# Optimization experiments

Measured on AMD Instinct MI355X. Metric: run time of the kernel, lower is better.

## Reference

```python
import jax, jax.numpy as jnp
import numpy as np

N_NODES = 50000
N_REL = 1000
N_EDGES = 600000
D = 128
DEPTH = 2


def setup_inputs() -> dict:
    key = jax.random.key(0)
    ks = jax.random.split(key, 10)
    features = jax.random.normal(ks[0], (N_NODES, D), dtype=jnp.float32)
    rel_emb = jax.random.normal(ks[1], (N_REL, D), dtype=jnp.float32)
    # edge list: row0 = destination (sorted, matches coalesced sparse layout), row1 = source
    dst = jnp.sort(jax.random.randint(ks[2], (N_EDGES,), 0, N_NODES))
    src = jax.random.randint(ks[3], (N_EDGES,), 0, N_NODES)
    adj = jnp.stack([dst, src]).astype(jnp.int64)
    # one relation entry per triple: r_index[0]=triple id, r_index[1]=relation id
    r_index = jnp.stack([
        jnp.arange(N_EDGES, dtype=jnp.int64),
        jax.random.randint(ks[4], (N_EDGES,), 0, N_REL).astype(jnp.int64),
    ])
    r_val = jax.random.uniform(ks[5], (N_EDGES,), dtype=jnp.float32)
    # Xavier-ish params
    attn_w = jax.random.normal(ks[6], (3 * D, 1), dtype=jnp.float32) * 0.05
    attn_b = jnp.zeros((1,), dtype=jnp.float32)
    gate_w = jax.random.normal(ks[7], (3 * D, 1), dtype=jnp.float32) * 0.05
    gate_b = jnp.zeros((1,), dtype=jnp.float32)
    attn_kernels = jax.random.normal(ks[8], (DEPTH, D, 1), dtype=jnp.float32) * (6.0 / (D + 1)) ** 0.5
    return {"features": features, "rel_emb": rel_emb, "adj": adj, "r_index": r_index,
            "r_val": r_val, "attn_w": attn_w, "attn_b": attn_b, "gate_w": gate_w,
            "gate_b": gate_b, "attn_kernels": attn_kernels}


def _segment_softmax(vals, seg, n):
    # numerically stable softmax over edges grouped by destination node `seg`
    m = jax.ops.segment_max(vals, seg, num_segments=n)
    e = jnp.exp(vals - m[seg])
    s = jax.ops.segment_sum(e, seg, num_segments=n)
    return e / s[seg]


def reference(features, rel_emb, adj, r_index, r_val, attn_w, attn_b, gate_w, gate_b, attn_kernels):
    n_nodes = features.shape[0]
    n_triples = adj.shape[1]
    depth = attn_kernels.shape[0]
    dst, src_idx = adj[0], adj[1]

    feats = jnp.tanh(features)
    outs_c = [feats]
    outs_s = [feats]

    for l in range(depth):
        # sparse [triple, rel] @ rel_emb -> per-triple relation embedding
        tri_rel = jax.ops.segment_sum(r_val[:, None] * rel_emb[r_index[1]], r_index[0],
                                      num_segments=n_triples)  # [E, D]
        tri_rel = tri_rel / jnp.maximum(
            jnp.linalg.norm(tri_rel, axis=1, keepdims=True), 1e-12)
        # gather neighbors and reflect through relation hyperplane
        neighs = feats[src_idx]  # [E, D]
        neighs = neighs - 2.0 * jnp.sum(neighs * tri_rel, axis=1, keepdims=True) * tri_rel
        # structural attention + row-wise sparse softmax
        att_struct = _segment_softmax((tri_rel @ attn_kernels[l])[:, 0], dst, n_nodes)
        feats = jnp.tanh(jax.ops.segment_sum(neighs * att_struct[:, None], dst,
                                             num_segments=n_nodes))
        outs_c.append(feats)
        # semantic branch on updated features
        neighs2 = feats[src_idx]
        source_emb = feats[dst]
        diff_raw = source_emb - neighs2
        att_input = jnp.concatenate([source_emb, neighs2, diff_raw], axis=-1)  # [E, 3D]
        att_score = jnp.maximum(jax.nn.sigmoid(att_input @ attn_w + attn_b)[:, 0], 1e-4)
        gate_score = jax.nn.sigmoid(att_input @ gate_w + gate_b)[:, 0]
        final_att = gate_score * att_score + (1.0 - gate_score) * att_struct
        att = _segment_softmax(final_att, dst, n_nodes)
        new_diff = jnp.tanh(jax.ops.segment_sum(diff_raw * att[:, None], dst,
                                                num_segments=n_nodes))
        outs_s.append(new_diff)

    return (jnp.concatenate(outs_c, axis=-1), jnp.concatenate(outs_s, axis=-1))
```

## Files before the change

### kernel.cpp

```cpp
#include <hip/hip_runtime.h>
#include <math.h>

#define N_NODES 50000
#define N_REL   1000
#define N_EDGES 600000
#define D       128
#define OUT_COLS 384

typedef unsigned short ushortT;

#define FEAT0_BLOCKS  ((N_NODES * (D / 4) + 255) / 256)
#define RELN_BLOCKS   ((N_REL + 3) / 4)
#define ROWPTR_BLOCKS ((N_NODES + 1 + 255) / 256)
#define SETUP_BLOCKS  (FEAT0_BLOCKS + RELN_BLOCKS + ROWPTR_BLOCKS + 1)

__device__ __forceinline__ float wave_reduce_sum64(float v) {
#pragma unroll
    for (int m = 1; m < 64; m <<= 1) v += __shfl_xor(v, m, 64);
    return v;
}

template <int CTRL>
__device__ __forceinline__ float dpp_add_(float v) {
    int t = __builtin_amdgcn_update_dpp(0, __float_as_int(v), CTRL, 0xf, 0xf, true);
    return v + __int_as_float(t);
}
__device__ __forceinline__ float group_sum16(float v) {
    v = dpp_add_<0xB1>(v);
    v = dpp_add_<0x4E>(v);
    v = dpp_add_<0x141>(v);
    v = dpp_add_<0x140>(v);
    return v;
}

__device__ __forceinline__ float tanh_fast(float x) {
    float cx = fminf(fmaxf(x, -20.0f), 20.0f);
    float e = __expf(2.0f * cx);
    return __fdividef(e - 1.0f, e + 1.0f);
}
__device__ __forceinline__ float sigmoid_fast(float x) {
    return __fdividef(1.0f, 1.0f + __expf(-x));
}

__device__ __forceinline__ void bf16x8_to_f32(uint4 q, float4& a, float4& b) {
    a.x = __int_as_float((int)(q.x << 16));
    a.y = __int_as_float((int)(q.x & 0xffff0000u));
    a.z = __int_as_float((int)(q.y << 16));
    a.w = __int_as_float((int)(q.y & 0xffff0000u));
    b.x = __int_as_float((int)(q.z << 16));
    b.y = __int_as_float((int)(q.z & 0xffff0000u));
    b.z = __int_as_float((int)(q.w << 16));
    b.w = __int_as_float((int)(q.w & 0xffff0000u));
}
__device__ __forceinline__ unsigned pack_bf16x2(float lo, float hi) {
    unsigned a = __float_as_uint(lo), b = __float_as_uint(hi);
    a = (a + 0x7fffu + ((a >> 16) & 1u)) >> 16;
    b = (b + 0x7fffu + ((b >> 16) & 1u));
    return (a & 0xffffu) | (b & 0xffff0000u);
}

__global__ __launch_bounds__(256) void k_setup(
        const float* __restrict__ features, const float* __restrict__ rel_emb,
        const float* __restrict__ attn_k, const float* __restrict__ attn_w,
        const float* __restrict__ gate_w, const int* __restrict__ dstv,
        float* __restrict__ out0, float* __restrict__ out1, ushortT* __restrict__ fc0,
        float* __restrict__ rel_norm, float* __restrict__ er0, float* __restrict__ er1,
        float* __restrict__ wcomb, int* __restrict__ row_ptr) {
    int bid = blockIdx.x, tid = threadIdx.x;
    if (bid < FEAT0_BLOCKS) {
        int i = bid * 256 + tid;
        if (i >= N_NODES * (D / 4)) return;
        int n = i >> 5, q = i & 31;
        float4 f = *(const float4*)(features + (size_t)n * D + 4 * q);
        f.x = tanh_fast(f.x); f.y = tanh_fast(f.y);
        f.z = tanh_fast(f.z); f.w = tanh_fast(f.w);
        *(float4*)(out0 + (size_t)n * OUT_COLS + 4 * q) = f;
        *(float4*)(out1 + (size_t)n * OUT_COLS + 4 * q) = f;
        uint2 p = make_uint2(pack_bf16x2(f.x, f.y), pack_bf16x2(f.z, f.w));
        *((uint2*)(fc0 + (size_t)n * D) + q) = p;
    } else if (bid < FEAT0_BLOCKS + RELN_BLOCKS) {
        int wid  = (bid - FEAT0_BLOCKS) * 4 + (tid >> 6);
        int lane = tid & 63;
        if (wid >= N_REL) return;
        float2 v = *(const float2*)(rel_emb + (size_t)wid * D + 2 * lane);
        float sq = wave_reduce_sum64(v.x * v.x + v.y * v.y);
        float inv = 1.0f / fmaxf(sqrtf(sq), 1e-12f);
        float2 u = make_float2(v.x * inv, v.y * inv);
        *(float2*)(rel_norm + (size_t)wid * D + 2 * lane) = u;
        float2 k0 = *(const float2*)(attn_k + 2 * lane);
        float2 k1 = *(const float2*)(attn_k + D + 2 * lane);
        float d0 = wave_reduce_sum64(u.x * k0.x + u.y * k0.y);
        float d1 = wave_reduce_sum64(u.x * k1.x + u.y * k1.y);
        if (lane == 0) { er0[wid] = __expf(d0); er1[wid] = __expf(d1); }
    } else if (bid < FEAT0_BLOCKS + RELN_BLOCKS + ROWPTR_BLOCKS) {
        int n = (bid - FEAT0_BLOCKS - RELN_BLOCKS) * 256 + tid;
        if (n > N_NODES) return;
        int lo = 0, hi = N_EDGES;
        while (lo < hi) {
            int mid = (lo + hi) >> 1;
            if (dstv[mid] < n) lo = mid + 1; else hi = mid;
        }
        row_ptr[n] = lo;
    } else {
        int j = tid;
        if (j >= D) return;
        wcomb[j]         = attn_w[j] + attn_w[2 * D + j];
        wcomb[D + j]     = attn_w[D + j] - attn_w[2 * D + j];
        wcomb[2 * D + j] = gate_w[j] + gate_w[2 * D + j];
        wcomb[3 * D + j] = gate_w[D + j] - gate_w[2 * D + j];
    }
}

__global__ __launch_bounds__(256) void k_struct(
        const ushortT* __restrict__ finC,
        ushortT* __restrict__ foutC,
        float* __restrict__ foutS,
        const int* __restrict__ row_ptr, const int* __restrict__ srcv,
        const int* __restrict__ relv, const float* __restrict__ rval,
        const float* __restrict__ er,
        const float* __restrict__ rel_norm, const float* __restrict__ wcomb,
        float* __restrict__ node_Z, float* __restrict__ proj) {
    int n    = (blockIdx.x * blockDim.x + threadIdx.x) >> 6;
    int lane = threadIdx.x & 63;
    int g = lane >> 4, l = lane & 15;
    if (n >= N_NODES) return;
    int beg = row_ptr[n], end = row_ptr[n + 1];

    float4 acc0 = make_float4(0.f, 0.f, 0.f, 0.f);
    float4 acc1 = make_float4(0.f, 0.f, 0.f, 0.f);
    float Zp = 0.f;

    for (int cs = beg; cs < end; cs += 64) {
        int cnt = min(64, end - cs);
        int my_s = 0, my_r = -1; float my_w = 0.f;
        if (lane < cnt) {
            int e = cs + lane;
            my_s = srcv[e];
            int rr = relv[e];
            bool pos = rval[e] > 0.0f;
            my_r = pos ? rr : -1;
            my_w = pos ? er[rr] : 1.0f;
            Zp += my_w;
        }
        int nit = (cnt + 3) >> 2;
        int   s = __shfl(my_s, g, 64);
        int   r = __shfl(my_r, g, 64);
        float w = __shfl(my_w, g, 64);
        uint4 xq = *((const uint4*)(finC + (size_t)s * D) + l);
        int rr0 = r < 0 ? 0 : r;
        const float* up = rel_norm + (size_t)rr0 * D + 8 * l;
        float4 u0 = *(const float4*)up;
        float4 u1 = *(const float4*)(up + 4);
        for (int i = 0; i < nit; ++i) {
            int r_c = r; float w_c = w;
            uint4 xq_c = xq; float4 u0_c = u0, u1_c = u1;
            if (i + 1 < nit) {
                int sl2 = ((i + 1) << 2) | g;
                s = __shfl(my_s, sl2, 64);
                r = __shfl(my_r, sl2, 64);
                w = __shfl(my_w, sl2, 64);
                xq = *((const uint4*)(finC + (size_t)s * D) + l);
                int rr2 = r < 0 ? 0 : r;
                const float* up2 = rel_norm + (size_t)rr2 * D + 8 * l;
                u0 = *(const float4*)up2;
                u1 = *(const float4*)(up2 + 4);
            }
            float4 x0, x1;
            bf16x8_to_f32(xq_c, x0, x1);
            float p = x0.x*u0_c.x + x0.y*u0_c.y + x0.z*u0_c.z + x0.w*u0_c.w
                    + x1.x*u1_c.x + x1.y*u1_c.y + x1.z*u1_c.z + x1.w*u1_c.w;
            p = group_sum16(p);
            float wc = (r_c >= 0) ? 2.0f * w_c * p : 0.0f;
            acc0.x += w_c * x0.x - wc * u0_c.x;
            acc0.y += w_c * x0.y - wc * u0_c.y;
            acc0.z += w_c * x0.z - wc * u0_c.z;
            acc0.w += w_c * x0.w - wc * u0_c.w;
            acc1.x += w_c * x1.x - wc * u1_c.x;
            acc1.y += w_c * x1.y - wc * u1_c.y;
            acc1.z += w_c * x1.z - wc * u1_c.z;
            acc1.w += w_c * x1.w - wc * u1_c.w;
        }
    }
    float Z = group_sum16(Zp);
    Z += __shfl_xor(Z, 16, 64);
    Z += __shfl_xor(Z, 32, 64);
#pragma unroll
    for (int m = 16; m < 64; m <<= 1) {
        acc0.x += __shfl_xor(acc0.x, m, 64);
        acc0.y += __shfl_xor(acc0.y, m, 64);
        acc0.z += __shfl_xor(acc0.z, m, 64);
        acc0.w += __shfl_xor(acc0.w, m, 64);
        acc1.x += __shfl_xor(acc1.x, m, 64);
        acc1.y += __shfl_xor(acc1.y, m, 64);
        acc1.z += __shfl_xor(acc1.z, m, 64);
        acc1.w += __shfl_xor(acc1.w, m, 64);
    }
    float invZ = (end > beg) ? (1.0f / Z) : 0.0f;
    float4 o0, o1;
    o0.x = tanh_fast(acc0.x * invZ); o0.y = tanh_fast(acc0.y * invZ);
    o0.z = tanh_fast(acc0.z * invZ); o0.w = tanh_fast(acc0.w * invZ);
    o1.x = tanh_fast(acc1.x * invZ); o1.y = tanh_fast(acc1.y * invZ);
    o1.z = tanh_fast(acc1.z * invZ); o1.w = tanh_fast(acc1.w * invZ);

    float pr[4];
#pragma unroll
    for (int k = 0; k < 4; ++k) {
        const float* wp = wcomb + k * D + 8 * l;
        float4 w0 = *(const float4*)wp;
        float4 w1 = *(const float4*)(wp + 4);
        float p = o0.x*w0.x + o0.y*w0.y + o0.z*w0.z + o0.w*w0.w
                + o1.x*w1.x + o1.y*w1.y + o1.z*w1.z + o1.w*w1.w;
        pr[k] = group_sum16(p);
    }
    if (lane == 0) {
        node_Z[n] = Z;
        *(float4*)(proj + 4 * (size_t)n) = make_float4(pr[0], pr[1], pr[2], pr[3]);
    }
    if (g == 0) {
        float* op = foutS + (size_t)n * OUT_COLS + 8 * l;
        *(float4*)op = o0;
        *(float4*)(op + 4) = o1;
        uint4 pk = make_uint4(pack_bf16x2(o0.x, o0.y), pack_bf16x2(o0.z, o0.w),
                              pack_bf16x2(o1.x, o1.y), pack_bf16x2(o1.z, o1.w));
        *((uint4*)(foutC + (size_t)n * D) + l) = pk;
    }
}

__global__ __launch_bounds__(256) void k_fused(
        const ushortT* __restrict__ finC,
        const float* __restrict__ seF,
        ushortT* __restrict__ foutC,
        float* __restrict__ foutS,
        float* __restrict__ oputSem,
        const int* __restrict__ row_ptr, const int* __restrict__ srcv,
        const int* __restrict__ relv, const float* __restrict__ rval,
        const float* __restrict__ er_sem,
        const float* __restrict__ er_st,
        const float* __restrict__ rel_norm, const float* __restrict__ wcomb,
        const float* __restrict__ node_Z0, const float* __restrict__ proj0,
        float* __restrict__ node_Z1, float* __restrict__ proj1,
        const float* __restrict__ attn_b, const float* __restrict__ gate_b) {
    int n    = (blockIdx.x * blockDim.x + threadIdx.x) >> 6;
    int lane = threadIdx.x & 63;
    int g = lane >> 4, l = lane & 15;
    if (n >= N_NODES) return;
    int beg = row_ptr[n], end = row_ptr[n + 1];

    float4 pn = *(const float4*)(proj0 + 4 * (size_t)n);
    float ca = pn.x + attn_b[0];
    float cg = pn.z + gate_b[0];
    float invZ0 = (end > beg) ? (1.0f / node_Z0[n]) : 0.0f;

    float4 st0 = make_float4(0.f, 0.f, 0.f, 0.f);
    float4 st1 = make_float4(0.f, 0.f, 0.f, 0.f);
    float4 sm0 = make_float4(0.f, 0.f, 0.f, 0.f);
    float4 sm1 = make_float4(0.f, 0.f, 0.f, 0.f);
    float Zp = 0.f, Zs = 0.f;

    for (int cs = beg; cs < end; cs += 64) {
        int cnt = min(64, end - cs);
        int my_s = 0, my_r = -1; float my_w = 0.f, my_wt = 0.f;
        if (lane < cnt) {
            int e = cs + lane;
            my_s = srcv[e];
            int rr = relv[e];
            bool pos = rval[e] > 0.0f;
            my_r = pos ? rr : -1;
            my_w = pos ? er_st[rr] : 1.0f;
            float sw = (pos ? er_sem[rr] : 1.0f) * invZ0;
            float4 ps = *(const float4*)(proj0 + 4 * (size_t)my_s);
            float as = fmaxf(sigmoid_fast(ca + ps.y), 1e-4f);
            float gt = sigmoid_fast(cg + ps.w);
            my_wt = __expf(gt * as + (1.0f - gt) * sw);
            Zp += my_w; Zs += my_wt;
        }
        int nit = (cnt + 3) >> 2;
        int   s  = __shfl(my_s, g, 64);
        int   r  = __shfl(my_r, g, 64);
        float w  = __shfl(my_w, g, 64);
        float wt = __shfl(my_wt, g, 64);
        uint4 xq = *((const uint4*)(finC + (size_t)s * D) + l);
        int rr0 = r < 0 ? 0 : r;
        const float* up = rel_norm + (size_t)rr0 * D + 8 * l;
        float4 u0 = *(const float4*)up;
        float4 u1 = *(const float4*)(up + 4);
        for (int i = 0; i < nit; ++i) {
            int r_c = r; float w_c = w, wt_c = wt;
            uint4 xq_c = xq; float4 u0_c = u0, u1_c = u1;
            if (i + 1 < nit) {
                int sl2 = ((i + 1) << 2) | g;
                s  = __shfl(my_s, sl2, 64);
                r  = __shfl(my_r, sl2, 64);
                w  = __shfl(my_w, sl2, 64);
                wt = __shfl(my_wt, sl2, 64);
                xq = *((const uint4*)(finC + (size_t)s * D) + l);
                int rr2 = r < 0 ? 0 : r;
                const float* up2 = rel_norm + (size_t)rr2 * D + 8 * l;
                u0 = *(const float4*)up2;
                u1 = *(const float4*)(up2 + 4);
            }
            float4 x0, x1;
            bf16x8_to_f32(xq_c, x0, x1);
            float p = x0.x*u0_c.x + x0.y*u0_c.y + x0.z*u0_c.z + x0.w*u0_c.w
                    + x1.x*u1_c.x + x1.y*u1_c.y + x1.z*u1_c.z + x1.w*u1_c.w;
            p = group_sum16(p);
            float wc = (r_c >= 0) ? 2.0f * w_c * p : 0.0f;
            st0.x += w_c * x0.x - wc * u0_c.x;
            st0.y += w_c * x0.y - wc * u0_c.y;
            st0.z += w_c * x0.z - wc * u0_c.z;
            st0.w += w_c * x0.w - wc * u0_c.w;
            st1.x += w_c * x1.x - wc * u1_c.x;
            st1.y += w_c * x1.y - wc * u1_c.y;
            st1.z += w_c * x1.z - wc * u1_c.z;
            st1.w += w_c * x1.w - wc * u1_c.w;
            sm0.x += wt_c * x0.x; sm0.y += wt_c * x0.y;
            sm0.z += wt_c * x0.z; sm0.w += wt_c * x0.w;
            sm1.x += wt_c * x1.x; sm1.y += wt_c * x1.y;
            sm1.z += wt_c * x1.z; sm1.w += wt_c * x1.w;
        }
    }
    float Z = group_sum16(Zp);
    Z += __shfl_xor(Z, 16, 64);
    Z += __shfl_xor(Z, 32, 64);
    float ZsT = group_sum16(Zs);
    ZsT += __shfl_xor(ZsT, 16, 64);
    ZsT += __shfl_xor(ZsT, 32, 64);
#pragma unroll
    for (int m = 16; m < 64; m <<= 1) {
        st0.x += __shfl_xor(st0.x, m, 64); st0.y += __shfl_xor(st0.y, m, 64);
        st0.z += __shfl_xor(st0.z, m, 64); st0.w += __shfl_xor(st0.w, m, 64);
        st1.x += __shfl_xor(st1.x, m, 64); st1.y += __shfl_xor(st1.y, m, 64);
        st1.z += __shfl_xor(st1.z, m, 64); st1.w += __shfl_xor(st1.w, m, 64);
        sm0.x += __shfl_xor(sm0.x, m, 64); sm0.y += __shfl_xor(sm0.y, m, 64);
        sm0.z += __shfl_xor(sm0.z, m, 64); sm0.w += __shfl_xor(sm0.w, m, 64);
        sm1.x += __shfl_xor(sm1.x, m, 64); sm1.y += __shfl_xor(sm1.y, m, 64);
        sm1.z += __shfl_xor(sm1.z, m, 64); sm1.w += __shfl_xor(sm1.w, m, 64);
    }
    float invZ = (end > beg) ? (1.0f / Z) : 0.0f;
    float4 o0, o1;
    o0.x = tanh_fast(st0.x * invZ); o0.y = tanh_fast(st0.y * invZ);
    o0.z = tanh_fast(st0.z * invZ); o0.w = tanh_fast(st0.w * invZ);
    o1.x = tanh_fast(st1.x * invZ); o1.y = tanh_fast(st1.y * invZ);
    o1.z = tanh_fast(st1.z * invZ); o1.w = tanh_fast(st1.w * invZ);

    float pr[4];
#pragma unroll
    for (int k = 0; k < 4; ++k) {
        const float* wp = wcomb + k * D + 8 * l;
        float4 w0 = *(const float4*)wp;
        float4 w1 = *(const float4*)(wp + 4);
        float p = o0.x*w0.x + o0.y*w0.y + o0.z*w0.z + o0.w*w0.w
                + o1.x*w1.x + o1.y*w1.y + o1.z*w1.z + o1.w*w1.w;
        pr[k] = group_sum16(p);
    }
    if (lane == 0) {
        node_Z1[n] = Z;
        *(float4*)(proj1 + 4 * (size_t)n) = make_float4(pr[0], pr[1], pr[2], pr[3]);
    }
    if (g == 0) {
        float* op = foutS + (size_t)n * OUT_COLS + 8 * l;
        *(float4*)op = o0;
        *(float4*)(op + 4) = o1;
        uint4 pk = make_uint4(pack_bf16x2(o0.x, o0.y), pack_bf16x2(o0.z, o0.w),
                              pack_bf16x2(o1.x, o1.y), pack_bf16x2(o1.z, o1.w));
        *((uint4*)(foutC + (size_t)n * D) + l) = pk;
        float invZs = (end > beg) ? (1.0f / ZsT) : 0.0f;
        float sc    = (end > beg) ? 1.0f : 0.0f;
        const float* sp = seF + (size_t)n * OUT_COLS + 8 * l;
        float4 s0 = *(const float4*)sp;
        float4 s1 = *(const float4*)(sp + 4);
        float4 q0, q1;
        q0.x = tanh_fast(sc * (s0.x - sm0.x * invZs));
        q0.y = tanh_fast(sc * (s0.y - sm0.y * invZs));
        q0.z = tanh_fast(sc * (s0.z - sm0.z * invZs));
        q0.w = tanh_fast(sc * (s0.w - sm0.w * invZs));
        q1.x = tanh_fast(sc * (s1.x - sm1.x * invZs));
        q1.y = tanh_fast(sc * (s1.y - sm1.y * invZs));
        q1.z = tanh_fast(sc * (s1.z - sm1.z * invZs));
        q1.w = tanh_fast(sc * (s1.w - sm1.w * invZs));
        float* oq = oputSem + (size_t)n * OUT_COLS + 8 * l;
        *(float4*)oq = q0;
        *(float4*)(oq + 4) = q1;
    }
}

__global__ __launch_bounds__(256) void k_sem(
        const ushortT* __restrict__ featsC,
        const float* __restrict__ seF,
        float* __restrict__ oput,
        const int* __restrict__ row_ptr, const int* __restrict__ srcv,
        const int* __restrict__ relv, const float* __restrict__ rval,
        const float* __restrict__ er, const float* __restrict__ node_Z,
        const float* __restrict__ proj,
        const float* __restrict__ attn_b, const float* __restrict__ gate_b) {
    int n    = (blockIdx.x * blockDim.x + threadIdx.x) >> 6;
    int lane = threadIdx.x & 63;
    int g = lane >> 4, l = lane & 15;
    if (n >= N_NODES) return;
    int beg = row_ptr[n], end = row_ptr[n + 1];

    float4 pn = *(const float4*)(proj + 4 * (size_t)n);
    float ca = pn.x + attn_b[0];
    float cg = pn.z + gate_b[0];
    float invZ = (end > beg) ? (1.0f / node_Z[n]) : 0.0f;

    float4 acc0 = make_float4(0.f, 0.f, 0.f, 0.f);
    float4 acc1 = make_float4(0.f, 0.f, 0.f, 0.f);
    float Zs = 0.f;

    for (int cs = beg; cs < end; cs += 64) {
        int cnt = min(64, end - cs);
        int my_s = 0; float my_wt = 0.f;
        if (lane < cnt) {
            int e = cs + lane;
            my_s = srcv[e];
            int rr = relv[e];
            bool pos = rval[e] > 0.0f;
            float sw = (pos ? er[rr] : 1.0f) * invZ;
            float4 ps = *(const float4*)(proj + 4 * (size_t)my_s);
            float as = fmaxf(sigmoid_fast(ca + ps.y), 1e-4f);
            float gt = sigmoid_fast(cg + ps.w);
            my_wt = __expf(gt * as + (1.0f - gt) * sw);
            Zs += my_wt;
        }
        int nit = (cnt + 3) >> 2;
        int   s  = __shfl(my_s, g, 64);
        float wt = __shfl(my_wt, g, 64);
        uint4 xq = *((const uint4*)(featsC + (size_t)s * D) + l);
        for (int i = 0; i < nit; ++i) {
            float wt_c = wt; uint4 xq_c = xq;
            if (i + 1 < nit) {
                int sl2 = ((i + 1) << 2) | g;
                s  = __shfl(my_s, sl2, 64);
                wt = __shfl(my_wt, sl2, 64);
                xq = *((const uint4*)(featsC + (size_t)s * D) + l);
            }
            float4 x0, x1;
            bf16x8_to_f32(xq_c, x0, x1);
            acc0.x += wt_c * x0.x; acc0.y += wt_c * x0.y;
            acc0.z += wt_c * x0.z; acc0.w += wt_c * x0.w;
            acc1.x += wt_c * x1.x; acc1.y += wt_c * x1.y;
            acc1.z += wt_c * x1.z; acc1.w += wt_c * x1.w;
        }
    }
    Zs = group_sum16(Zs);
    Zs += __shfl_xor(Zs, 16, 64);
    Zs += __shfl_xor(Zs, 32, 64);
#pragma unroll
    for (int m = 16; m < 64; m <<= 1) {
        acc0.x += __shfl_xor(acc0.x, m, 64);
        acc0.y += __shfl_xor(acc0.y, m, 64);
        acc0.z += __shfl_xor(acc0.z, m, 64);
        acc0.w += __shfl_xor(acc0.w, m, 64);
        acc1.x += __shfl_xor(acc1.x, m, 64);
        acc1.y += __shfl_xor(acc1.y, m, 64);
        acc1.z += __shfl_xor(acc1.z, m, 64);
        acc1.w += __shfl_xor(acc1.w, m, 64);
    }
    if (g == 0) {
        float invZs = (end > beg) ? (1.0f / Zs) : 0.0f;
        float sc    = (end > beg) ? 1.0f : 0.0f;
        const float* sp = seF + (size_t)n * OUT_COLS + 8 * l;
        float4 s0 = *(const float4*)sp;
        float4 s1 = *(const float4*)(sp + 4);
        float4 o0, o1;
        o0.x = tanh_fast(sc * (s0.x - acc0.x * invZs));
        o0.y = tanh_fast(sc * (s0.y - acc0.y * invZs));
        o0.z = tanh_fast(sc * (s0.z - acc0.z * invZs));
        o0.w = tanh_fast(sc * (s0.w - acc0.w * invZs));
        o1.x = tanh_fast(sc * (s1.x - acc1.x * invZs));
        o1.y = tanh_fast(sc * (s1.y - acc1.y * invZs));
        o1.z = tanh_fast(sc * (s1.z - acc1.z * invZs));
        o1.w = tanh_fast(sc * (s1.w - acc1.w * invZs));
        float* op = oput + (size_t)n * OUT_COLS + 8 * l;
        *(float4*)op = o0;
        *(float4*)(op + 4) = o1;
    }
}

extern "C" void kernel_launch(void* const* d_in, const int* in_sizes, int n_in,
                              void* d_out, int out_size, void* d_ws, size_t ws_size,
                              hipStream_t stream) {
    const float* features = (const float*)d_in[0];
    const float* rel_emb  = (const float*)d_in[1];
    const int*   adj      = (const int*)d_in[2];
    const int*   r_index  = (const int*)d_in[3];
    const float* r_val    = (const float*)d_in[4];
    const float* attn_w   = (const float*)d_in[5];
    const float* attn_b   = (const float*)d_in[6];
    const float* gate_w   = (const float*)d_in[7];
    const float* gate_b   = (const float*)d_in[8];
    const float* attn_k   = (const float*)d_in[9];

    float* out0 = (float*)d_out;
    float* out1 = out0 + (size_t)N_NODES * OUT_COLS;

    float* rel_norm = (float*)d_ws;
    float* er0      = rel_norm + (size_t)N_REL * D;
    float* er1      = er0 + N_REL;
    float* wcomb    = er1 + N_REL;
    float* proj0    = wcomb + 4 * D;
    float* proj1    = proj0 + 4 * (size_t)N_NODES;
    float* node_Z0  = proj1 + 4 * (size_t)N_NODES;
    float* node_Z1  = node_Z0 + N_NODES;
    int*   row_ptr  = (int*)(node_Z1 + N_NODES);
    ushortT* fc0    = (ushortT*)(row_ptr + N_NODES + 4);
    ushortT* fc1    = fc0 + (size_t)N_NODES * D;
    ushortT* fc2    = fc1 + (size_t)N_NODES * D;

    const int* dstv = adj;
    const int* srcv = adj + N_EDGES;
    const int* relv = r_index + N_EDGES;

    k_setup<<<SETUP_BLOCKS, 256, 0, stream>>>(
        features, rel_emb, attn_k, attn_w, gate_w, dstv,
        out0, out1, fc0, rel_norm, er0, er1, wcomb, row_ptr);

    k_struct<<<(N_NODES + 3) / 4, 256, 0, stream>>>(
        fc0, fc1, out0 + (size_t)1 * D,
        row_ptr, srcv, relv, r_val, er0, rel_norm, wcomb, node_Z0, proj0);

    k_fused<<<(N_NODES + 3) / 4, 256, 0, stream>>>(
        fc1, out0 + (size_t)1 * D, fc2, out0 + (size_t)2 * D, out1 + (size_t)1 * D,
        row_ptr, srcv, relv, r_val, er0, er1, rel_norm, wcomb,
        node_Z0, proj0, node_Z1, proj1, attn_b, gate_b);

    k_sem<<<(N_NODES + 3) / 4, 256, 0, stream>>>(
        fc2, out0 + (size_t)2 * D, out1 + (size_t)2 * D,
        row_ptr, srcv, relv, r_val, er1, node_Z1, proj1, attn_b, gate_b);
}
```

Baseline: 360.6 us.

## Fuse four kernels into one persistent kernel with software grid barriers

Replaces the setup, struct, fused and sem kernel launches with a single persistent kernel of 960 blocks. Each phase is processed with grid-stride loops over nodes, one wave per node, and the phases are separated by atomic-counter grid barriers. The intent is to remove kernel launch gaps and tail effects between dependent phases. The costs are spin-wait overhead, fixed occupancy limits, and a deadlock risk if all 960 blocks cannot be co-resident. An extra memset is needed to reset the barrier counters on every call.

Measured after the change: 1.244 ms. 245% more time.

```diff
diff --git a/kernel.cpp b/kernel.cpp
--- a/kernel.cpp
+++ b/kernel.cpp
@@ -7,12 +7,12 @@
 #define D       128
 #define OUT_COLS 384
 
+#define NBLOCKS  960
+#define NTHREADS 256
+#define NWAVES   (NBLOCKS * NTHREADS / 64)
+#define NTHR     (NBLOCKS * NTHREADS)
+
 typedef unsigned short ushortT;
-
-#define FEAT0_BLOCKS  ((N_NODES * (D / 4) + 255) / 256)
-#define RELN_BLOCKS   ((N_REL + 3) / 4)
-#define ROWPTR_BLOCKS ((N_NODES + 1 + 255) / 256)
-#define SETUP_BLOCKS  (FEAT0_BLOCKS + RELN_BLOCKS + ROWPTR_BLOCKS + 1)
 
 __device__ __forceinline__ float wave_reduce_sum64(float v) {
 #pragma unroll
@@ -59,71 +59,28 @@
     return (a & 0xffffu) | (b & 0xffff0000u);
 }
 
-__global__ __launch_bounds__(256) void k_setup(
-        const float* __restrict__ features, const float* __restrict__ rel_emb,
-        const float* __restrict__ attn_k, const float* __restrict__ attn_w,
-        const float* __restrict__ gate_w, const int* __restrict__ dstv,
-        float* __restrict__ out0, float* __restrict__ out1, ushortT* __restrict__ fc0,
-        float* __restrict__ rel_norm, float* __restrict__ er0, float* __restrict__ er1,
-        float* __restrict__ wcomb, int* __restrict__ row_ptr) {
-    int bid = blockIdx.x, tid = threadIdx.x;
-    if (bid < FEAT0_BLOCKS) {
-        int i = bid * 256 + tid;
-        if (i >= N_NODES * (D / 4)) return;
-        int n = i >> 5, q = i & 31;
-        float4 f = *(const float4*)(features + (size_t)n * D + 4 * q);
-        f.x = tanh_fast(f.x); f.y = tanh_fast(f.y);
-        f.z = tanh_fast(f.z); f.w = tanh_fast(f.w);
-        *(float4*)(out0 + (size_t)n * OUT_COLS + 4 * q) = f;
-        *(float4*)(out1 + (size_t)n * OUT_COLS + 4 * q) = f;
-        uint2 p = make_uint2(pack_bf16x2(f.x, f.y), pack_bf16x2(f.z, f.w));
-        *((uint2*)(fc0 + (size_t)n * D) + q) = p;
-    } else if (bid < FEAT0_BLOCKS + RELN_BLOCKS) {
-        int wid  = (bid - FEAT0_BLOCKS) * 4 + (tid >> 6);
-        int lane = tid & 63;
-        if (wid >= N_REL) return;
-        float2 v = *(const float2*)(rel_emb + (size_t)wid * D + 2 * lane);
-        float sq = wave_reduce_sum64(v.x * v.x + v.y * v.y);
-        float inv = 1.0f / fmaxf(sqrtf(sq), 1e-12f);
-        float2 u = make_float2(v.x * inv, v.y * inv);
-        *(float2*)(rel_norm + (size_t)wid * D + 2 * lane) = u;
-        float2 k0 = *(const float2*)(attn_k + 2 * lane);
-        float2 k1 = *(const float2*)(attn_k + D + 2 * lane);
-        float d0 = wave_reduce_sum64(u.x * k0.x + u.y * k0.y);
-        float d1 = wave_reduce_sum64(u.x * k1.x + u.y * k1.y);
-        if (lane == 0) { er0[wid] = __expf(d0); er1[wid] = __expf(d1); }
-    } else if (bid < FEAT0_BLOCKS + RELN_BLOCKS + ROWPTR_BLOCKS) {
-        int n = (bid - FEAT0_BLOCKS - RELN_BLOCKS) * 256 + tid;
-        if (n > N_NODES) return;
-        int lo = 0, hi = N_EDGES;
-        while (lo < hi) {
-            int mid = (lo + hi) >> 1;
-            if (dstv[mid] < n) lo = mid + 1; else hi = mid;
-        }
-        row_ptr[n] = lo;
-    } else {
-        int j = tid;
-        if (j >= D) return;
-        wcomb[j]         = attn_w[j] + attn_w[2 * D + j];
-        wcomb[D + j]     = attn_w[D + j] - attn_w[2 * D + j];
-        wcomb[2 * D + j] = gate_w[j] + gate_w[2 * D + j];
-        wcomb[3 * D + j] = gate_w[D + j] - gate_w[2 * D + j];
-    }
-}
-
-__global__ __launch_bounds__(256) void k_struct(
-        const ushortT* __restrict__ finC,
-        ushortT* __restrict__ foutC,
+__device__ __forceinline__ void grid_sync(int* bar, int phase) {
+    __syncthreads();
+    if (threadIdx.x == 0) {
+        __hip_atomic_fetch_add(bar + phase, 1, __ATOMIC_RELEASE, __HIP_MEMORY_SCOPE_AGENT);
+        while (__hip_atomic_load(bar + phase, __ATOMIC_ACQUIRE, __HIP_MEMORY_SCOPE_AGENT) < NBLOCKS) {
+            __builtin_amdgcn_s_sleep(2);
+        }
+    }
+    __syncthreads();
+}
+
+
+__device__ __forceinline__ void do_struct(
+        int n, int lane,
+        const ushortT* __restrict__ finC, ushortT* __restrict__ foutC,
         float* __restrict__ foutS,
         const int* __restrict__ row_ptr, const int* __restrict__ srcv,
         const int* __restrict__ relv, const float* __restrict__ rval,
         const float* __restrict__ er,
         const float* __restrict__ rel_norm, const float* __restrict__ wcomb,
         float* __restrict__ node_Z, float* __restrict__ proj) {
-    int n    = (blockIdx.x * blockDim.x + threadIdx.x) >> 6;
-    int lane = threadIdx.x & 63;
     int g = lane >> 4, l = lane & 15;
-    if (n >= N_NODES) return;
     int beg = row_ptr[n], end = row_ptr[n + 1];
 
     float4 acc0 = make_float4(0.f, 0.f, 0.f, 0.f);
@@ -226,24 +183,19 @@
     }
 }
 
-__global__ __launch_bounds__(256) void k_fused(
-        const ushortT* __restrict__ finC,
-        const float* __restrict__ seF,
-        ushortT* __restrict__ foutC,
-        float* __restrict__ foutS,
+__device__ __forceinline__ void do_fused(
+        int n, int lane,
+        const ushortT* __restrict__ finC, const float* __restrict__ seF,
+        ushortT* __restrict__ foutC, float* __restrict__ foutS,
         float* __restrict__ oputSem,
         const int* __restrict__ row_ptr, const int* __restrict__ srcv,
         const int* __restrict__ relv, const float* __restrict__ rval,
-        const float* __restrict__ er_sem,
-        const float* __restrict__ er_st,
+        const float* __restrict__ er_sem, const float* __restrict__ er_st,
         const float* __restrict__ rel_norm, const float* __restrict__ wcomb,
         const float* __restrict__ node_Z0, const float* __restrict__ proj0,
         float* __restrict__ node_Z1, float* __restrict__ proj1,
         const float* __restrict__ attn_b, const float* __restrict__ gate_b) {
-    int n    = (blockIdx.x * blockDim.x + threadIdx.x) >> 6;
-    int lane = threadIdx.x & 63;
     int g = lane >> 4, l = lane & 15;
-    if (n >= N_NODES) return;
     int beg = row_ptr[n], end = row_ptr[n + 1];
 
     float4 pn = *(const float4*)(proj0 + 4 * (size_t)n);
@@ -384,19 +336,16 @@
     }
 }
 
-__global__ __launch_bounds__(256) void k_sem(
-        const ushortT* __restrict__ featsC,
-        const float* __restrict__ seF,
+__device__ __forceinline__ void do_sem(
+        int n, int lane,
+        const ushortT* __restrict__ featsC, const float* __restrict__ seF,
         float* __restrict__ oput,
         const int* __restrict__ row_ptr, const int* __restrict__ srcv,
         const int* __restrict__ relv, const float* __restrict__ rval,
         const float* __restrict__ er, const float* __restrict__ node_Z,
         const float* __restrict__ proj,
         const float* __restrict__ attn_b, const float* __restrict__ gate_b) {
-    int n    = (blockIdx.x * blockDim.x + threadIdx.x) >> 6;
-    int lane = threadIdx.x & 63;
     int g = lane >> 4, l = lane & 15;
-    if (n >= N_NODES) return;
     int beg = row_ptr[n], end = row_ptr[n + 1];
 
     float4 pn = *(const float4*)(proj + 4 * (size_t)n);
@@ -478,6 +427,80 @@
     }
 }
 
+__global__ __launch_bounds__(NTHREADS, 4) void k_mega(
+        const float* __restrict__ features, const float* __restrict__ rel_emb,
+        const float* __restrict__ attn_k, const float* __restrict__ attn_w,
+        const float* __restrict__ gate_w,
+        const float* __restrict__ attn_b, const float* __restrict__ gate_b,
+        const int* __restrict__ dstv, const int* __restrict__ srcv,
+        const int* __restrict__ relv, const float* __restrict__ rval,
+        float* __restrict__ out0, float* __restrict__ out1,
+        float* __restrict__ rel_norm, float* __restrict__ er0, float* __restrict__ er1,
+        float* __restrict__ wcomb,
+        float* __restrict__ proj0, float* __restrict__ proj1,
+        float* __restrict__ node_Z0, float* __restrict__ node_Z1,
+        int* __restrict__ row_ptr,
+        ushortT* __restrict__ fc0, ushortT* __restrict__ fc1, ushortT* __restrict__ fc2,
+        int* __restrict__ bar) {
+    int gtid = blockIdx.x * NTHREADS + threadIdx.x;
+    int lane = threadIdx.x & 63;
+    int wid  = gtid >> 6;
+
+    for (int i = gtid; i < N_NODES * (D / 4); i += NTHR) {
+        int n = i >> 5, q = i & 31;
+        float4 f = *(const float4*)(features + (size_t)n * D + 4 * q);
+        f.x = tanh_fast(f.x); f.y = tanh_fast(f.y);
+        f.z = tanh_fast(f.z); f.w = tanh_fast(f.w);
+        *(float4*)(out0 + (size_t)n * OUT_COLS + 4 * q) = f;
+        *(float4*)(out1 + (size_t)n * OUT_COLS + 4 * q) = f;
+        uint2 p = make_uint2(pack_bf16x2(f.x, f.y), pack_bf16x2(f.z, f.w));
+        *((uint2*)(fc0 + (size_t)n * D) + q) = p;
+    }
+    for (int r = wid; r < N_REL; r += NWAVES) {
+        float2 v = *(const float2*)(rel_emb + (size_t)r * D + 2 * lane);
+        float sq = wave_reduce_sum64(v.x * v.x + v.y * v.y);
+        float inv = 1.0f / fmaxf(sqrtf(sq), 1e-12f);
+        float2 u = make_float2(v.x * inv, v.y * inv);
+        *(float2*)(rel_norm + (size_t)r * D + 2 * lane) = u;
+        float2 k0 = *(const float2*)(attn_k + 2 * lane);
+        float2 k1 = *(const float2*)(attn_k + D + 2 * lane);
+        float d0 = wave_reduce_sum64(u.x * k0.x + u.y * k0.y);
+        float d1 = wave_reduce_sum64(u.x * k1.x + u.y * k1.y);
+        if (lane == 0) { er0[r] = __expf(d0); er1[r] = __expf(d1); }
+    }
+    for (int n = gtid; n <= N_NODES; n += NTHR) {
+        int lo = 0, hi = N_EDGES;
+        while (lo < hi) {
+            int mid = (lo + hi) >> 1;
+            if (dstv[mid] < n) lo = mid + 1; else hi = mid;
+        }
+        row_ptr[n] = lo;
+    }
+    if (gtid < D) {
+        int j = gtid;
+        wcomb[j]         = attn_w[j] + attn_w[2 * D + j];
+        wcomb[D + j]     = attn_w[D + j] - attn_w[2 * D + j];
+        wcomb[2 * D + j] = gate_w[j] + gate_w[2 * D + j];
+        wcomb[3 * D + j] = gate_w[D + j] - gate_w[2 * D + j];
+    }
+    grid_sync(bar, 0);
+
+    for (int n = wid; n < N_NODES; n += NWAVES)
+        do_struct(n, lane, fc0, fc1, out0 + D, row_ptr, srcv, relv, rval,
+                  er0, rel_norm, wcomb, node_Z0, proj0);
+    grid_sync(bar, 1);
+
+    for (int n = wid; n < N_NODES; n += NWAVES)
+        do_fused(n, lane, fc1, out0 + D, fc2, out0 + 2 * D, out1 + D,
+                 row_ptr, srcv, relv, rval, er0, er1, rel_norm, wcomb,
+                 node_Z0, proj0, node_Z1, proj1, attn_b, gate_b);
+    grid_sync(bar, 2);
+
+    for (int n = wid; n < N_NODES; n += NWAVES)
+        do_sem(n, lane, fc2, out0 + 2 * D, out1 + 2 * D,
+               row_ptr, srcv, relv, rval, er1, node_Z1, proj1, attn_b, gate_b);
+}
+
 extern "C" void kernel_launch(void* const* d_in, const int* in_sizes, int n_in,
                               void* d_out, int out_size, void* d_ws, size_t ws_size,
                               hipStream_t stream) {
@@ -495,7 +518,8 @@
     float* out0 = (float*)d_out;
     float* out1 = out0 + (size_t)N_NODES * OUT_COLS;
 
-    float* rel_norm = (float*)d_ws;
+    int*   bar      = (int*)d_ws;
+    float* rel_norm = (float*)d_ws + 16;
     float* er0      = rel_norm + (size_t)N_REL * D;
     float* er1      = er0 + N_REL;
     float* wcomb    = er1 + N_REL;
@@ -512,20 +536,11 @@
     const int* srcv = adj + N_EDGES;
     const int* relv = r_index + N_EDGES;
 
-    k_setup<<<SETUP_BLOCKS, 256, 0, stream>>>(
-        features, rel_emb, attn_k, attn_w, gate_w, dstv,
-        out0, out1, fc0, rel_norm, er0, er1, wcomb, row_ptr);
-
-    k_struct<<<(N_NODES + 3) / 4, 256, 0, stream>>>(
-        fc0, fc1, out0 + (size_t)1 * D,
-        row_ptr, srcv, relv, r_val, er0, rel_norm, wcomb, node_Z0, proj0);
-
-    k_fused<<<(N_NODES + 3) / 4, 256, 0, stream>>>(
-        fc1, out0 + (size_t)1 * D, fc2, out0 + (size_t)2 * D, out1 + (size_t)1 * D,
-        row_ptr, srcv, relv, r_val, er0, er1, rel_norm, wcomb,
-        node_Z0, proj0, node_Z1, proj1, attn_b, gate_b);
-
-    k_sem<<<(N_NODES + 3) / 4, 256, 0, stream>>>(
-        fc2, out0 + (size_t)2 * D, out1 + (size_t)2 * D,
-        row_ptr, srcv, relv, r_val, er1, node_Z1, proj1, attn_b, gate_b);
-}
+    hipMemsetAsync(bar, 0, 64, stream);
+
+    k_mega<<<NBLOCKS, NTHREADS, 0, stream>>>(
+        features, rel_emb, attn_k, attn_w, gate_w, attn_b, gate_b,
+        dstv, srcv, relv, r_val,
+        out0, out1, rel_norm, er0, er1, wcomb,
+        proj0, proj1, node_Z0, node_Z1, row_ptr, fc0, fc1, fc2, bar);
+}
```
